# Optimization experiments

Hardware: AMD Instinct MI355X
Metric: run time of the kernel (lower is better)

## Reference

```python
import jax, jax.numpy as jnp
import numpy as np

B, T, N, D = 16, 12, 1024, 64
E = 32          # num hyperedges
DEPTH = 3
WIN = 2         # window_size
EPS = 1e-5      # torch LayerNorm default


def setup_inputs() -> dict:
    key = jax.random.key(0)
    ks = jax.random.split(key, 8)
    return {
        "x": jax.random.normal(ks[0], (B, T, N, D), jnp.float32),
        "W1": jax.random.normal(ks[1], (DEPTH, D, D), jnp.float32) / np.float32(np.sqrt(D)),
        "b1": jax.random.normal(ks[2], (DEPTH, D), jnp.float32) * 0.02,
        "W2": jax.random.normal(ks[3], (DEPTH, D, D), jnp.float32) / np.float32(np.sqrt(D)),
        "b2": jax.random.normal(ks[4], (DEPTH, D), jnp.float32) * 0.02,
        "ln_g": jnp.ones((DEPTH, D), jnp.float32),
        "ln_b": jnp.zeros((DEPTH, D), jnp.float32),
        "edge_clf": jax.random.normal(ks[5], (D, E), jnp.float32) / np.float32(np.sqrt(E)),
        "edge_map": jax.random.normal(ks[6], (E, E), jnp.float32) / np.float32(np.sqrt(E)),
        "hg": jnp.ones((D,), jnp.float32),
        "hb": jnp.zeros((D,), jnp.float32),
    }


def _layer_norm(h, g, b):
    m = jnp.mean(h, axis=-1, keepdims=True)
    v = jnp.mean(jnp.square(h - m), axis=-1, keepdims=True)
    return (h - m) * jax.lax.rsqrt(v + EPS) * g + b


def _stgcn(x, W1, b1, W2, b2, g, bta, A):
    pad = jnp.zeros((B, WIN - 1, N, D), x.dtype)
    fp = jnp.concatenate([pad, x], axis=1)
    large = jnp.concatenate([fp[:, i:i + T] for i in range(WIN)], axis=2)
    z1 = jnp.einsum('btmd,od->btmo', large, W1) + b1
    z2 = jnp.einsum('btmd,od->btmo', large, W2) + b2
    g1 = jnp.einsum('nm,btmd->btnd', A, z1)                    # (B,T,N,D)
    g2 = jnp.einsum('nm,btmd->btnd', A, z2)
    h = jax.nn.relu(g1 * g2) + g1
    return _layer_norm(h + x, g, bta)


def _hyper(x, edge_clf, edge_map, hg, hb):
    feat = x.reshape(B, T * N, D)                              # (B, M, D)
    assign = jax.nn.softmax(feat @ edge_clf, axis=-1)          # (B, M, E)
    hyper_feat = jnp.einsum('bme,bmd->bed', assign, feat)      # (B, E, D)
    hyper_mapped = jax.nn.relu(jnp.einsum('ef,bfd->bed', edge_map, hyper_feat))
    hyper_out = hyper_mapped + hyper_feat
    y = jax.nn.relu(jnp.einsum('bme,bed->bmd', assign, hyper_out)).reshape(x.shape)
    return _layer_norm(y + x, hg, hb)


def reference(x, W1, b1, W2, b2, ln_g, ln_b, edge_clf, edge_map, hg, hb):
    # expanded_adj: faithful to source — the eye-repeat assignment overwrites adj,
    A = jnp.tile(jnp.eye(N, dtype=x.dtype), (1, WIN)) / WIN
    for i in range(DEPTH):
        out1 = _stgcn(x, W1[i], b1[i], W2[i], b2[i], ln_g[i], ln_b[i], A)
        out2 = _hyper(x, edge_clf, edge_map, hg, hb)
        x = (out1 + out2) * 0.5
        # dropout is identity in eval mode
    return x
```

## Files before the change

kernel.cpp:

```cpp
#include <hip/hip_runtime.h>

#define BB 16
#define TT 12
#define NN 1024
#define DD 64
#define EE 32
#define MM (TT*NN)
#define ROWS (BB*MM)
#define CPB2N 96
#define S_ITER (384/(CPB2N*4))
#define CPB4 64
#define LN_EPS 1e-5f

typedef __attribute__((ext_vector_type(8))) short short8;
typedef __attribute__((ext_vector_type(4))) float f32x4;
typedef __attribute__((ext_vector_type(4))) int   int4v;

__device__ __forceinline__ int cvt2(float a, float b){
  int r;
  asm("v_cvt_pk_bf16_f32 %0, %1, %2" : "=v"(r) : "v"(a), "v"(b));
  return r;
}
__device__ __forceinline__ unsigned short bf16of(float a){
  return (unsigned short)(cvt2(a, a) & 0xffff);
}
__device__ __forceinline__ float f32of(unsigned short h){
  return __builtin_bit_cast(float, (unsigned int)h << 16);
}
__device__ __forceinline__ float lo16f(int w){ return __builtin_bit_cast(float, (unsigned int)w << 16); }
__device__ __forceinline__ float hi16f(int w){ return __builtin_bit_cast(float, (unsigned int)w & 0xffff0000u); }

__device__ __forceinline__ short8 pack_hi8(const float* v){
  int4v w;
  w.x = cvt2(v[0], v[1]); w.y = cvt2(v[2], v[3]);
  w.z = cvt2(v[4], v[5]); w.w = cvt2(v[6], v[7]);
  return __builtin_bit_cast(short8, w);
}
__device__ __forceinline__ short8 pack_lo8(const float* v, short8 hi){
  const int4v wh = __builtin_bit_cast(int4v, hi);
  float r[8];
  r[0] = v[0] - lo16f(wh.x); r[1] = v[1] - hi16f(wh.x);
  r[2] = v[2] - lo16f(wh.y); r[3] = v[3] - hi16f(wh.y);
  r[4] = v[4] - lo16f(wh.z); r[5] = v[5] - hi16f(wh.z);
  r[6] = v[6] - lo16f(wh.w); r[7] = v[7] - hi16f(wh.w);
  return pack_hi8(r);
}

__global__ __launch_bounds__(256, 3)
void k2_hyper1(const float* __restrict__ x, const float* __restrict__ clf,
               unsigned short* __restrict__ assign_hi, unsigned short* __restrict__ assign_lo,
               float* __restrict__ hf_part)
{
  __shared__ __align__(16) float lbuf[4224];
  const int lane = threadIdx.x & 63;
  const int wid  = threadIdx.x >> 6;
  const int l15  = lane & 15;
  const int lg   = lane >> 4;
  const int b    = blockIdx.x / CPB2N;
  const int blk  = blockIdx.x % CPB2N;
  float* amat = lbuf + wid*1056;

  short8 bch[2][2], bcl[2][2];
  #pragma unroll
  for (int kc = 0; kc < 2; ++kc)
    #pragma unroll
    for (int nt = 0; nt < 2; ++nt){
      float v[8];
      #pragma unroll
      for (int j = 0; j < 8; ++j)
        v[j] = clf[(size_t)(32*kc + 8*lg + j)*EE + 16*nt + l15];
      bch[kc][nt] = pack_hi8(v);
      bcl[kc][nt] = pack_lo8(v, bch[kc][nt]);
    }

  f32x4 acc2[2][4];
  #pragma unroll
  for (int et = 0; et < 2; ++et)
    #pragma unroll
    for (int dt = 0; dt < 4; ++dt) acc2[et][dt] = (f32x4){0.f,0.f,0.f,0.f};

  const int wslot = blk*4 + wid;
  #pragma unroll 1
  for (int s = 0; s < S_ITER; ++s){
    const int c = wslot + s*(CPB2N*4);
    const size_t grb = (size_t)b*MM + (size_t)c*32;

    #pragma unroll 1
    for (int h = 0; h < 2; ++h){
      short8 axh[2], axl[2];
      #pragma unroll
      for (int kc = 0; kc < 2; ++kc){
        const float* p = x + (grb + 16*h + l15)*DD + 32*kc + 8*lg;
        float v[8];
        const float4 p0 = *reinterpret_cast<const float4*>(p);
        const float4 p1 = *reinterpret_cast<const float4*>(p + 4);
        v[0]=p0.x; v[1]=p0.y; v[2]=p0.z; v[3]=p0.w;
        v[4]=p1.x; v[5]=p1.y; v[6]=p1.z; v[7]=p1.w;
        axh[kc] = pack_hi8(v); axl[kc] = pack_lo8(v, axh[kc]);
      }
      f32x4 accL[2] = {(f32x4){0.f,0.f,0.f,0.f},(f32x4){0.f,0.f,0.f,0.f}};
      #pragma unroll
      for (int kc = 0; kc < 2; ++kc)
        #pragma unroll
        for (int nt = 0; nt < 2; ++nt){
          accL[nt] = __builtin_amdgcn_mfma_f32_16x16x32_bf16(axh[kc], bch[kc][nt], accL[nt], 0, 0, 0);
          accL[nt] = __builtin_amdgcn_mfma_f32_16x16x32_bf16(axh[kc], bcl[kc][nt], accL[nt], 0, 0, 0);
          accL[nt] = __builtin_amdgcn_mfma_f32_16x16x32_bf16(axl[kc], bch[kc][nt], accL[nt], 0, 0, 0);
        }
      #pragma unroll
      for (int q = 0; q < 4; ++q){
        const float l0 = accL[0][q], l1 = accL[1][q];
        float mx = fmaxf(l0, l1);
        #pragma unroll
        for (int off = 8; off; off >>= 1) mx = fmaxf(mx, __shfl_xor(mx, off));
        const float e0 = expf(l0 - mx), e1 = expf(l1 - mx);
        float sm = e0 + e1;
        #pragma unroll
        for (int off = 8; off; off >>= 1) sm += __shfl_xor(sm, off);
        const float inv = 1.f / sm;
        const float a0 = e0*inv, a1 = e1*inv;
        const int rloc = 16*h + 4*lg + q;
        const size_t row = grb + rloc;
        const unsigned short h0 = bf16of(a0);
        const unsigned short h1 = bf16of(a1);
        assign_hi[row*EE + l15]      = h0;
        assign_hi[row*EE + 16 + l15] = h1;
        assign_lo[row*EE + l15]      = bf16of(a0 - f32of(h0));
        assign_lo[row*EE + 16 + l15] = bf16of(a1 - f32of(h1));
        amat[rloc*33 + l15]      = a0;
        amat[rloc*33 + 16 + l15] = a1;
      }
    }
    __builtin_amdgcn_wave_barrier();
    short8 a2h[2], a2l[2];
    #pragma unroll
    for (int et = 0; et < 2; ++et){
      float v[8];
      #pragma unroll
      for (int j = 0; j < 8; ++j)
        v[j] = amat[(8*lg + j)*33 + 16*et + l15];
      a2h[et] = pack_hi8(v); a2l[et] = pack_lo8(v, a2h[et]);
    }
    #pragma unroll
    for (int dt = 0; dt < 4; ++dt){
      float v[8];
      #pragma unroll
      for (int j = 0; j < 8; ++j)
        v[j] = x[(grb + 8*lg + j)*DD + 16*dt + l15];
      const short8 b2 = pack_hi8(v);
      #pragma unroll
      for (int et = 0; et < 2; ++et){
        acc2[et][dt] = __builtin_amdgcn_mfma_f32_16x16x32_bf16(a2h[et], b2, acc2[et][dt], 0, 0, 0);
        acc2[et][dt] = __builtin_amdgcn_mfma_f32_16x16x32_bf16(a2l[et], b2, acc2[et][dt], 0, 0, 0);
      }
    }
    __builtin_amdgcn_wave_barrier();
  }

  __syncthreads();
  float* red = lbuf;
  if (wid < 2){
    #pragma unroll
    for (int et = 0; et < 2; ++et)
      #pragma unroll
      for (int dt = 0; dt < 4; ++dt)
        #pragma unroll
        for (int q = 0; q < 4; ++q)
          red[wid*2080 + (16*et + 4*lg + q)*65 + 16*dt + l15] = acc2[et][dt][q];
  }
  __syncthreads();
  if (wid >= 2){
    #pragma unroll
    for (int et = 0; et < 2; ++et)
      #pragma unroll
      for (int dt = 0; dt < 4; ++dt)
        #pragma unroll
        for (int q = 0; q < 4; ++q)
          red[(wid-2)*2080 + (16*et + 4*lg + q)*65 + 16*dt + l15] += acc2[et][dt][q];
  }
  __syncthreads();
  float* dst = hf_part + ((size_t)b*CPB2N + blk)*(EE*DD);
  for (int i = threadIdx.x; i < EE*DD; i += 256){
    const int e = i >> 6, d = i & 63;
    dst[i] = red[e*65 + d] + red[2080 + e*65 + d];
  }
}

__global__ void k3_edge(const float* __restrict__ hf_part, const float* __restrict__ em,
                        unsigned short* __restrict__ ho_hi, unsigned short* __restrict__ ho_lo)
{
  __shared__ float ems[EE*EE];
  __shared__ float hfs[EE*DD];
  const int b = blockIdx.x;
  const int tid = threadIdx.x;
  for (int i = tid; i < EE*EE; i += 256) ems[i] = em[i];
  for (int i = tid; i < EE*DD; i += 256){
    const float* p = hf_part + (size_t)b*CPB2N*(EE*DD) + i;
    float s0=0.f, s1=0.f, s2=0.f, s3=0.f;
    #pragma unroll
    for (int k = 0; k < CPB2N; k += 4){
      s0 += p[(size_t)(k+0)*EE*DD]; s1 += p[(size_t)(k+1)*EE*DD];
      s2 += p[(size_t)(k+2)*EE*DD]; s3 += p[(size_t)(k+3)*EE*DD];
    }
    hfs[i] = (s0+s1)+(s2+s3);
  }
  __syncthreads();
  for (int i = tid; i < EE*DD; i += 256){
    const int e = i >> 6, d = i & 63;
    float acc = 0.f;
    #pragma unroll
    for (int f = 0; f < EE; ++f) acc = fmaf(ems[e*EE+f], hfs[f*DD+d], acc);
    const float v = fmaxf(acc, 0.f) + hfs[e*DD+d];
    const unsigned short hi = bf16of(v);
    const unsigned short lo = bf16of(v - f32of(hi));
    ho_hi[((size_t)b*DD + d)*EE + e] = hi;
    ho_lo[((size_t)b*DD + d)*EE + e] = lo;
  }
}

__global__ __launch_bounds__(256, 2)
void k14_fused(const float* __restrict__ x,
               const float* __restrict__ W1, const float* __restrict__ b1,
               const float* __restrict__ W2, const float* __restrict__ b2,
               const float* __restrict__ lng, const float* __restrict__ lnb,
               const unsigned short* __restrict__ assign_hi,
               const unsigned short* __restrict__ assign_lo,
               const unsigned short* __restrict__ ho_hi,
               const unsigned short* __restrict__ ho_lo,
               const float* __restrict__ hg, const float* __restrict__ hb,
               float* __restrict__ xout)
{
  const int lane = threadIdx.x & 63;
  const int wid  = threadIdx.x >> 6;
  const int b    = blockIdx.x / CPB4;
  const int blk  = blockIdx.x % CPB4;
  const int l15  = lane & 15;
  const int lg   = lane >> 4;
  const int k0   = lg * 8;

  short8 bw[2][4][2];
  const float* Wm[2] = {W1, W2};
  #pragma unroll
  for (int m = 0; m < 2; ++m)
    #pragma unroll
    for (int nt = 0; nt < 4; ++nt)
      #pragma unroll
      for (int kc = 0; kc < 2; ++kc){
        const float* src = Wm[m] + (size_t)(16*nt + l15)*DD + 32*kc + k0;
        const float4 p0 = *reinterpret_cast<const float4*>(src);
        const float4 p1 = *reinterpret_cast<const float4*>(src + 4);
        int4v w;
        w.x = cvt2(p0.x, p0.y); w.y = cvt2(p0.z, p0.w);
        w.z = cvt2(p1.x, p1.y); w.w = cvt2(p1.z, p1.w);
        bw[m][nt][kc] = __builtin_bit_cast(short8, w);
      }

  short8 bwh[4], bwl[4];
  #pragma unroll
  for (int nt = 0; nt < 4; ++nt){
    const size_t off = ((size_t)b*DD + l15 + 16*nt)*EE + 8*lg;
    bwh[nt] = *reinterpret_cast<const short8*>(ho_hi + off);
    bwl[nt] = *reinterpret_cast<const short8*>(ho_lo + off);
  }

  float b1c[4], b2c[4], g1c[4], B1c[4], g2c[4], B2c[4];
  #pragma unroll
  for (int nt = 0; nt < 4; ++nt){
    b1c[nt] = b1[l15 + 16*nt];
    b2c[nt] = b2[l15 + 16*nt];
    g1c[nt] = lng[l15 + 16*nt];
    B1c[nt] = lnb[l15 + 16*nt];
    g2c[nt] = hg[l15 + 16*nt];
    B2c[nt] = hb[l15 + 16*nt];
  }

  const int tpb = MM / 16;
  for (int tl = blk*4 + wid; tl < tpb; tl += CPB4*4){
    const size_t r0 = (size_t)b*MM + (size_t)tl*16;
    const int t = (tl*16) >> 10;

    const float* pc = x + (r0 + l15)*DD + k0;
    float4 a00 = *reinterpret_cast<const float4*>(pc);
    float4 a01 = *reinterpret_cast<const float4*>(pc + 4);
    float4 a10 = *reinterpret_cast<const float4*>(pc + 32);
    float4 a11 = *reinterpret_cast<const float4*>(pc + 36);
    if (t > 0){
      const float* pp = pc - (size_t)NN*DD;
      const float4 q00 = *reinterpret_cast<const float4*>(pp);
      const float4 q01 = *reinterpret_cast<const float4*>(pp + 4);
      const float4 q10 = *reinterpret_cast<const float4*>(pp + 32);
      const float4 q11 = *reinterpret_cast<const float4*>(pp + 36);
      a00.x = 0.5f*(a00.x+q00.x); a00.y = 0.5f*(a00.y+q00.y);
      a00.z = 0.5f*(a00.z+q00.z); a00.w = 0.5f*(a00.w+q00.w);
      a01.x = 0.5f*(a01.x+q01.x); a01.y = 0.5f*(a01.y+q01.y);
      a01.z = 0.5f*(a01.z+q01.z); a01.w = 0.5f*(a01.w+q01.w);
      a10.x = 0.5f*(a10.x+q10.x); a10.y = 0.5f*(a10.y+q10.y);
      a10.z = 0.5f*(a10.z+q10.z); a10.w = 0.5f*(a10.w+q10.w);
      a11.x = 0.5f*(a11.x+q11.x); a11.y = 0.5f*(a11.y+q11.y);
      a11.z = 0.5f*(a11.z+q11.z); a11.w = 0.5f*(a11.w+q11.w);
    } else {
      a00.x*=0.5f;a00.y*=0.5f;a00.z*=0.5f;a00.w*=0.5f;
      a01.x*=0.5f;a01.y*=0.5f;a01.z*=0.5f;a01.w*=0.5f;
      a10.x*=0.5f;a10.y*=0.5f;a10.z*=0.5f;a10.w*=0.5f;
      a11.x*=0.5f;a11.y*=0.5f;a11.z*=0.5f;a11.w*=0.5f;
    }
    float epi[4][4];
    #pragma unroll
    for (int q = 0; q < 4; ++q){
      const float* pr = x + (r0 + 4*lg + q)*DD + l15;
      #pragma unroll
      for (int nt = 0; nt < 4; ++nt) epi[q][nt] = pr[16*nt];
    }
    const short8 afh = *reinterpret_cast<const short8*>(assign_hi + (r0 + l15)*EE + 8*lg);
    const short8 afl = *reinterpret_cast<const short8*>(assign_lo + (r0 + l15)*EE + 8*lg);

    short8 af[2];
    {
      int4v w;
      w.x = cvt2(a00.x, a00.y); w.y = cvt2(a00.z, a00.w);
      w.z = cvt2(a01.x, a01.y); w.w = cvt2(a01.z, a01.w);
      af[0] = __builtin_bit_cast(short8, w);
      w.x = cvt2(a10.x, a10.y); w.y = cvt2(a10.z, a10.w);
      w.z = cvt2(a11.x, a11.y); w.w = cvt2(a11.z, a11.w);
      af[1] = __builtin_bit_cast(short8, w);
    }

    f32x4 acc1[2][4], acc4[4];
    #pragma unroll
    for (int m = 0; m < 2; ++m)
      #pragma unroll
      for (int nt = 0; nt < 4; ++nt) acc1[m][nt] = (f32x4){0.f,0.f,0.f,0.f};
    #pragma unroll
    for (int nt = 0; nt < 4; ++nt) acc4[nt] = (f32x4){0.f,0.f,0.f,0.f};

    #pragma unroll
    for (int kc = 0; kc < 2; ++kc){
      #pragma unroll
      for (int nt = 0; nt < 4; ++nt){
        acc1[0][nt] = __builtin_amdgcn_mfma_f32_16x16x32_bf16(af[kc], bw[0][nt][kc], acc1[0][nt], 0, 0, 0);
        acc1[1][nt] = __builtin_amdgcn_mfma_f32_16x16x32_bf16(af[kc], bw[1][nt][kc], acc1[1][nt], 0, 0, 0);
      }
    }
    #pragma unroll
    for (int nt = 0; nt < 4; ++nt){
      acc4[nt] = __builtin_amdgcn_mfma_f32_16x16x32_bf16(afh, bwh[nt], acc4[nt], 0, 0, 0);
      acc4[nt] = __builtin_amdgcn_mfma_f32_16x16x32_bf16(afh, bwl[nt], acc4[nt], 0, 0, 0);
      acc4[nt] = __builtin_amdgcn_mfma_f32_16x16x32_bf16(afl, bwh[nt], acc4[nt], 0, 0, 0);
    }

    #pragma unroll
    for (int q = 0; q < 4; ++q){
      const size_t row = r0 + 4*lg + q;
      float s1[4], s2[4];
      float rs1 = 0.f, rs2 = 0.f;
      #pragma unroll
      for (int nt = 0; nt < 4; ++nt){
        const float g1 = acc1[0][nt][q] + b1c[nt];
        const float g2 = acc1[1][nt][q] + b2c[nt];
        s1[nt] = fmaxf(g1*g2, 0.f) + g1 + epi[q][nt];
        rs1 += s1[nt];
        s2[nt] = fmaxf(acc4[nt][q], 0.f) + epi[q][nt];
        rs2 += s2[nt];
      }
      #pragma unroll
      for (int off = 8; off; off >>= 1){ rs1 += __shfl_xor(rs1, off); rs2 += __shfl_xor(rs2, off); }
      const float m1 = rs1 * (1.f/DD);
      const float m2 = rs2 * (1.f/DD);
      float d1[4], d2[4]; float v1 = 0.f, v2 = 0.f;
      #pragma unroll
      for (int nt = 0; nt < 4; ++nt){
        d1[nt] = s1[nt] - m1; v1 = fmaf(d1[nt], d1[nt], v1);
        d2[nt] = s2[nt] - m2; v2 = fmaf(d2[nt], d2[nt], v2);
      }
      #pragma unroll
      for (int off = 8; off; off >>= 1){ v1 += __shfl_xor(v1, off); v2 += __shfl_xor(v2, off); }
      const float i1 = rsqrtf(v1 * (1.f/DD) + LN_EPS);
      const float i2 = rsqrtf(v2 * (1.f/DD) + LN_EPS);
      #pragma unroll
      for (int nt = 0; nt < 4; ++nt){
        const float o1 = d1[nt]*i1*g1c[nt] + B1c[nt];
        const float o2 = d2[nt]*i2*g2c[nt] + B2c[nt];
        xout[row*DD + l15 + 16*nt] = 0.5f*(o1 + o2);
      }
    }
  }
}

extern "C" void kernel_launch(void* const* d_in, const int* in_sizes, int n_in,
                              void* d_out, int out_size, void* d_ws, size_t ws_size,
                              hipStream_t stream)
{
  (void)in_sizes; (void)n_in; (void)out_size; (void)ws_size;
  const float* x0  = (const float*)d_in[0];
  const float* W1  = (const float*)d_in[1];
  const float* b1  = (const float*)d_in[2];
  const float* W2  = (const float*)d_in[3];
  const float* b2  = (const float*)d_in[4];
  const float* lng = (const float*)d_in[5];
  const float* lnb = (const float*)d_in[6];
  const float* clf = (const float*)d_in[7];
  const float* em  = (const float*)d_in[8];
  const float* hg  = (const float*)d_in[9];
  const float* hb  = (const float*)d_in[10];
  float* out = (float*)d_out;

  float* ws_x = (float*)d_ws;
  float* hf_part = ws_x + (size_t)ROWS*DD;
  unsigned short* assign_hi = (unsigned short*)(hf_part + (size_t)BB*CPB2N*EE*DD);
  unsigned short* assign_lo = assign_hi + (size_t)ROWS*EE;
  unsigned short* ho_hi     = assign_lo + (size_t)ROWS*EE;
  unsigned short* ho_lo     = ho_hi + (size_t)BB*DD*EE;

  const float* xin_seq[3]  = { x0, out, ws_x };
  float*       xout_seq[3] = { out, ws_x, out };

  for (int i = 0; i < 3; ++i){
    const float* xin = xin_seq[i];
    float* xout = xout_seq[i];
    k2_hyper1<<<BB*CPB2N, 256, 0, stream>>>(xin, clf, assign_hi, assign_lo, hf_part);
    k3_edge<<<BB, 256, 0, stream>>>(hf_part, em, ho_hi, ho_lo);
    k14_fused<<<BB*CPB4, 256, 0, stream>>>(xin, W1 + i*DD*DD, b1 + i*DD,
                                           W2 + i*DD*DD, b2 + i*DD,
                                           lng + i*DD, lnb + i*DD,
                                           assign_hi, assign_lo, ho_hi, ho_lo,
                                           hg, hb, xout);
  }
}
```

Measured before the change: 263.6 us.

## Replace partial-sum buffer and edge kernel with atomics and fused edge mapping

The hyperedge feature reduction now uses float atomicAdd into a zeroed per-batch buffer, where before each block wrote a partial tile that a separate kernel summed. The small edge-mapping kernel is removed. Its matmul, relu and residual are recomputed redundantly in every block of the fused main kernel, then split into hi/lo bf16 operands there. This saves one launch and the partial-sum round trip per layer, at the cost of a memset launch, atomic contention, extra shared memory that may lower occupancy, and nondeterministic summation order.

```diff
diff --git a/kernel.cpp b/kernel.cpp
--- a/kernel.cpp
+++ b/kernel.cpp
@@ -49,7 +49,7 @@
 __global__ __launch_bounds__(256, 3)
 void k2_hyper1(const float* __restrict__ x, const float* __restrict__ clf,
                unsigned short* __restrict__ assign_hi, unsigned short* __restrict__ assign_lo,
-               float* __restrict__ hf_part)
+               float* __restrict__ hf)
 {
   __shared__ __align__(16) float lbuf[4224];
   const int lane = threadIdx.x & 63;
@@ -179,42 +179,9 @@
           red[(wid-2)*2080 + (16*et + 4*lg + q)*65 + 16*dt + l15] += acc2[et][dt][q];
   }
   __syncthreads();
-  float* dst = hf_part + ((size_t)b*CPB2N + blk)*(EE*DD);
   for (int i = threadIdx.x; i < EE*DD; i += 256){
     const int e = i >> 6, d = i & 63;
-    dst[i] = red[e*65 + d] + red[2080 + e*65 + d];
-  }
-}
-
-__global__ void k3_edge(const float* __restrict__ hf_part, const float* __restrict__ em,
-                        unsigned short* __restrict__ ho_hi, unsigned short* __restrict__ ho_lo)
-{
-  __shared__ float ems[EE*EE];
-  __shared__ float hfs[EE*DD];
-  const int b = blockIdx.x;
-  const int tid = threadIdx.x;
-  for (int i = tid; i < EE*EE; i += 256) ems[i] = em[i];
-  for (int i = tid; i < EE*DD; i += 256){
-    const float* p = hf_part + (size_t)b*CPB2N*(EE*DD) + i;
-    float s0=0.f, s1=0.f, s2=0.f, s3=0.f;
-    #pragma unroll
-    for (int k = 0; k < CPB2N; k += 4){
-      s0 += p[(size_t)(k+0)*EE*DD]; s1 += p[(size_t)(k+1)*EE*DD];
-      s2 += p[(size_t)(k+2)*EE*DD]; s3 += p[(size_t)(k+3)*EE*DD];
-    }
-    hfs[i] = (s0+s1)+(s2+s3);
-  }
-  __syncthreads();
-  for (int i = tid; i < EE*DD; i += 256){
-    const int e = i >> 6, d = i & 63;
-    float acc = 0.f;
-    #pragma unroll
-    for (int f = 0; f < EE; ++f) acc = fmaf(ems[e*EE+f], hfs[f*DD+d], acc);
-    const float v = fmaxf(acc, 0.f) + hfs[e*DD+d];
-    const unsigned short hi = bf16of(v);
-    const unsigned short lo = bf16of(v - f32of(hi));
-    ho_hi[((size_t)b*DD + d)*EE + e] = hi;
-    ho_lo[((size_t)b*DD + d)*EE + e] = lo;
+    atomicAdd(&hf[(size_t)b*EE*DD + i], red[e*65 + d] + red[2080 + e*65 + d]);
   }
 }
 
@@ -225,11 +192,13 @@
                const float* __restrict__ lng, const float* __restrict__ lnb,
                const unsigned short* __restrict__ assign_hi,
                const unsigned short* __restrict__ assign_lo,
-               const unsigned short* __restrict__ ho_hi,
-               const unsigned short* __restrict__ ho_lo,
+               const float* __restrict__ hf, const float* __restrict__ em,
                const float* __restrict__ hg, const float* __restrict__ hb,
                float* __restrict__ xout)
 {
+  __shared__ float ems[EE*EE];
+  __shared__ float hfs[EE*DD];
+  __shared__ float hos[EE*DD];
   const int lane = threadIdx.x & 63;
   const int wid  = threadIdx.x >> 6;
   const int b    = blockIdx.x / CPB4;
@@ -237,6 +206,29 @@
   const int l15  = lane & 15;
   const int lg   = lane >> 4;
   const int k0   = lg * 8;
+
+  for (int i = threadIdx.x; i < EE*EE; i += 256) ems[i] = em[i];
+  for (int i = threadIdx.x; i < EE*DD; i += 256) hfs[i] = hf[(size_t)b*EE*DD + i];
+  __syncthreads();
+  for (int i = threadIdx.x; i < EE*DD; i += 256){
+    const int e = i >> 6, d = i & 63;
+    float acc = 0.f;
+    #pragma unroll
+    for (int f = 0; f < EE; ++f) acc = fmaf(ems[e*EE+f], hfs[f*DD+d], acc);
+    hos[i] = fmaxf(acc, 0.f) + hfs[e*DD+d];
+  }
+  __syncthreads();
+
+  short8 bwh[4], bwl[4];
+  #pragma unroll
+  for (int nt = 0; nt < 4; ++nt){
+    float v[8];
+    #pragma unroll
+    for (int j = 0; j < 8; ++j)
+      v[j] = hos[(8*lg + j)*DD + l15 + 16*nt];
+    bwh[nt] = pack_hi8(v);
+    bwl[nt] = pack_lo8(v, bwh[nt]);
+  }
 
   short8 bw[2][4][2];
   const float* Wm[2] = {W1, W2};
@@ -254,14 +246,6 @@
         w.z = cvt2(p1.x, p1.y); w.w = cvt2(p1.z, p1.w);
         bw[m][nt][kc] = __builtin_bit_cast(short8, w);
       }
-
-  short8 bwh[4], bwl[4];
-  #pragma unroll
-  for (int nt = 0; nt < 4; ++nt){
-    const size_t off = ((size_t)b*DD + l15 + 16*nt)*EE + 8*lg;
-    bwh[nt] = *reinterpret_cast<const short8*>(ho_hi + off);
-    bwl[nt] = *reinterpret_cast<const short8*>(ho_lo + off);
-  }
 
   float b1c[4], b2c[4], g1c[4], B1c[4], g2c[4], B2c[4];
   #pragma unroll
@@ -405,11 +389,9 @@
   float* out = (float*)d_out;
 
   float* ws_x = (float*)d_ws;
-  float* hf_part = ws_x + (size_t)ROWS*DD;
-  unsigned short* assign_hi = (unsigned short*)(hf_part + (size_t)BB*CPB2N*EE*DD);
+  float* hf   = ws_x + (size_t)ROWS*DD;
+  unsigned short* assign_hi = (unsigned short*)(hf + (size_t)BB*EE*DD);
   unsigned short* assign_lo = assign_hi + (size_t)ROWS*EE;
-  unsigned short* ho_hi     = assign_lo + (size_t)ROWS*EE;
-  unsigned short* ho_lo     = ho_hi + (size_t)BB*DD*EE;
 
   const float* xin_seq[3]  = { x0, out, ws_x };
   float*       xout_seq[3] = { out, ws_x, out };
@@ -417,12 +399,12 @@
   for (int i = 0; i < 3; ++i){
     const float* xin = xin_seq[i];
     float* xout = xout_seq[i];
-    k2_hyper1<<<BB*CPB2N, 256, 0, stream>>>(xin, clf, assign_hi, assign_lo, hf_part);
-    k3_edge<<<BB, 256, 0, stream>>>(hf_part, em, ho_hi, ho_lo);
+    hipMemsetAsync(hf, 0, (size_t)BB*EE*DD*sizeof(float), stream);
+    k2_hyper1<<<BB*CPB2N, 256, 0, stream>>>(xin, clf, assign_hi, assign_lo, hf);
     k14_fused<<<BB*CPB4, 256, 0, stream>>>(xin, W1 + i*DD*DD, b1 + i*DD,
                                            W2 + i*DD*DD, b2 + i*DD,
                                            lng + i*DD, lnb + i*DD,
-                                           assign_hi, assign_lo, ho_hi, ho_lo,
+                                           assign_hi, assign_lo, hf, em,
                                            hg, hb, xout);
   }
 }
```

Measured after the change: 224.1 us. -15.0%, faster.
